# Optimization experiments

Hardware: AMD Instinct MI355X
Metric: run time of the kernel (lower is better)

Reference implementation:

```python
import jax, jax.numpy as jnp
import numpy as np

N_NODES = 50000
N_EDGES = 800000
D_IN = 256
D_HID = 128


def setup_inputs() -> dict:
    key = jax.random.key(0)
    ks = jax.random.split(key, 10)
    x = jax.random.normal(ks[0], (N_NODES, D_IN), dtype=jnp.float32)
    edge_index = jax.random.randint(ks[1], (2, N_EDGES), 0, N_NODES, dtype=jnp.int64)
    # GCNConv params (glorot-ish init), 3 layers: 256->128, 128->128, 128->128
    def glorot(k, fan_in, fan_out):
        s = jnp.sqrt(6.0 / (fan_in + fan_out))
        return jax.random.uniform(k, (fan_in, fan_out), jnp.float32, -s, s)
    W0 = glorot(ks[2], D_IN, D_HID)
    b0 = jnp.zeros((D_HID,), jnp.float32)
    W1 = glorot(ks[3], D_HID, D_HID)
    b1 = jnp.zeros((D_HID,), jnp.float32)
    W2 = glorot(ks[4], D_HID, D_HID)
    b2 = jnp.zeros((D_HID,), jnp.float32)
    return {"x": x, "edge_index": edge_index, "W0": W0, "b0": b0,
            "W1": W1, "b1": b1, "W2": W2, "b2": b2}


def _gcn_conv(x, W, b, src, dst, deg_inv_sqrt, deg_inv):
    # PyG GCNConv: x' = D^{-1/2} (A + I) D^{-1/2} (x W) + b
    h = x @ W  # [N, d_out]
    norm = deg_inv_sqrt[src] * deg_inv_sqrt[dst]  # [E]
    msg = h[src] * norm[:, None]  # gather + scale, [E, d_out]
    agg = jax.ops.segment_sum(msg, dst, num_segments=x.shape[0])
    # self-loop contribution: norm = deg^{-1/2} * deg^{-1/2} = 1/deg
    return agg + h * deg_inv[:, None] + b


def reference(x, edge_index, W0, b0, W1, b1, W2, b2):
    src, dst = edge_index[0], edge_index[1]
    n = x.shape[0]
    # degree with self loops (computed on destination, source_to_target flow)
    deg = jax.ops.segment_sum(jnp.ones((src.shape[0],), x.dtype), dst,
                              num_segments=n) + 1.0
    deg_inv_sqrt = deg ** -0.5
    deg_inv = 1.0 / deg
    h = jax.nn.relu(_gcn_conv(x, W0, b0, src, dst, deg_inv_sqrt, deg_inv))
    h = jax.nn.relu(_gcn_conv(h, W1, b1, src, dst, deg_inv_sqrt, deg_inv))
    h = jax.nn.relu(_gcn_conv(h, W2, b2, src, dst, deg_inv_sqrt, deg_inv))
    return h
```

## Files before the change

### kernel.cpp

```cpp
#include <hip/hip_runtime.h>

#define N_NODES 50000
#define N_EDGES 800000
#define D_HID   128

typedef unsigned int uint;
typedef unsigned short ushort;
typedef __attribute__((ext_vector_type(8))) short short8;
typedef __attribute__((ext_vector_type(4))) float f32x4;

#define NB       196
#define CAP      6144
#define P1_BLOCKS 200
#define P1_CHUNK  4000

__global__ __launch_bounds__(256) void part_k(const int* __restrict__ src,
                                              const int* __restrict__ dst,
                                              int* __restrict__ bcur,
                                              int2* __restrict__ ebuf, int e) {
    __shared__ int hist[NB];
    __shared__ int base[NB];
    int tid = threadIdx.x;
    if (tid < NB) hist[tid] = 0;
    __syncthreads();

    int e0 = blockIdx.x * P1_CHUNK;
    int2 ed[16];
    bool val[16];
#pragma unroll
    for (int i = 0; i < 16; ++i) {
        int o = i * 256 + tid;
        int idx = e0 + o;
        val[i] = (o < P1_CHUNK) && (idx < e);
        if (val[i]) {
            ed[i] = make_int2(src[idx], dst[idx]);
            atomicAdd(&hist[ed[i].y >> 8], 1);
        }
    }
    __syncthreads();
    if (tid < NB && hist[tid] > 0) base[tid] = atomicAdd(&bcur[tid], hist[tid]);
    __syncthreads();
    if (tid < NB) hist[tid] = 0;
    __syncthreads();
#pragma unroll
    for (int i = 0; i < 16; ++i) {
        if (val[i]) {
            int bk = ed[i].y >> 8;
            int o  = base[bk] + atomicAdd(&hist[bk], 1);
            if (o < CAP) ebuf[(size_t)bk * CAP + o] = ed[i];
        }
    }
}

__global__ void bscan196_k(const int* __restrict__ bcur, int* __restrict__ boff,
                           int* __restrict__ row_ptr_end) {
    __shared__ int s[256];
    int t = threadIdx.x;
    int v = (t < NB) ? bcur[t] : 0;
    s[t] = v;
    __syncthreads();
    for (int off = 1; off < 256; off <<= 1) {
        int u = (t >= off) ? s[t - off] : 0;
        __syncthreads();
        s[t] += u;
        __syncthreads();
    }
    if (t < NB) boff[t] = s[t] - v;
    if (t == 255) *row_ptr_end = s[255];
}

__global__ __launch_bounds__(256) void cntscan_k(const int2* __restrict__ ebuf,
                                                 const int* __restrict__ bcnt,
                                                 const int* __restrict__ boff,
                                                 int* __restrict__ row_ptr,
                                                 float* __restrict__ dis, int n) {
    __shared__ int c[256];
    __shared__ int s[256];
    int b = blockIdx.x, tid = threadIdx.x;
    c[tid] = 0;
    __syncthreads();
    int m = bcnt[b]; if (m > CAP) m = CAP;
    for (int i = tid; i < m; i += 256)
        atomicAdd(&c[ebuf[(size_t)b * CAP + i].y & 255], 1);
    __syncthreads();
    int v = c[tid];
    s[tid] = v;
    __syncthreads();
    for (int off = 1; off < 256; off <<= 1) {
        int u = (tid >= off) ? s[tid - off] : 0;
        __syncthreads();
        s[tid] += u;
        __syncthreads();
    }
    int node = b * 256 + tid;
    if (node < n) {
        row_ptr[node] = boff[b] + s[tid] - v;
        dis[node] = rsqrtf((float)v + 1.0f);
    }
}

__global__ __launch_bounds__(256) void csr_k(const int2* __restrict__ ebuf,
                                             const int* __restrict__ bcnt,
                                             const int* __restrict__ row_ptr,
                                             int* __restrict__ col, int n) {
    __shared__ int rp_l[257];
    __shared__ int cur[256];
    __shared__ int win[CAP];
    int b = blockIdx.x, tid = threadIdx.x;
    int node0 = b * 256;
    for (int i = tid; i < 257; i += 256) {
        int nd = node0 + i; if (nd > n) nd = n;
        rp_l[i] = row_ptr[nd];
    }
    cur[tid] = 0;
    __syncthreads();
    int base0 = rp_l[0];
    int m = bcnt[b]; if (m > CAP) m = CAP;

    for (int i = tid; i < m; i += 256) {
        int2 ed = ebuf[(size_t)b * CAP + i];
        int ll = ed.y & 255;
        int pos = rp_l[ll] + atomicAdd(&cur[ll], 1) - base0;
        win[pos] = ed.x << 8;
    }
    __syncthreads();
    for (int i = tid; i < m; i += 256) col[base0 + i] = win[i];
}

__global__ __launch_bounds__(256) void rowsort_k(const int* __restrict__ rp,
                                                 int* __restrict__ col, int n) {
    int node = blockIdx.x * 4 + (threadIdx.x >> 6);
    if (node >= n) return;
    int lane = threadIdx.x & 63;
    int beg = rp[node], end = rp[node + 1];
    int len = end - beg;
    if (len <= 1) return;
    if (len <= 64) {
        int v = (lane < len) ? col[beg + lane] : 0x7fffffff;
#pragma unroll
        for (int k = 2; k <= 64; k <<= 1)
#pragma unroll
            for (int j = k >> 1; j > 0; j >>= 1) {
                int other = __shfl_xor(v, j);
                bool up    = (lane & k) == 0;
                bool small = (lane & j) == 0;
                v = (small == up) ? min(v, other) : max(v, other);
            }
        if (lane < len) col[beg + lane] = v;
    } else if (lane == 0) {
        for (int i = beg + 1; i < end; ++i) {
            int key = col[i]; int j = i - 1;
            while (j >= beg && col[j] > key) { col[j + 1] = col[j]; --j; }
            col[j + 1] = key;
        }
    }
}

__device__ inline ushort f2bf(float f) {
    unsigned u = __float_as_uint(f);
    unsigned rounding = 0x7fffu + ((u >> 16) & 1u);
    return (ushort)((u + rounding) >> 16);
}
__device__ inline float bf_lo(uint v) { return __uint_as_float(v << 16); }
__device__ inline float bf_hi(uint v) { return __uint_as_float(v & 0xffff0000u); }
__device__ inline short8 cvt8(float4 f0, float4 f1) {
    short8 r;
    r[0] = (short)f2bf(f0.x); r[1] = (short)f2bf(f0.y);
    r[2] = (short)f2bf(f0.z); r[3] = (short)f2bf(f0.w);
    r[4] = (short)f2bf(f1.x); r[5] = (short)f2bf(f1.y);
    r[6] = (short)f2bf(f1.z); r[7] = (short)f2bf(f1.w);
    return r;
}

__device__ inline void gload16(const void* g, void* l) {
    __builtin_amdgcn_global_load_lds(
        (const __attribute__((address_space(1))) uint*)g,
        (__attribute__((address_space(3))) uint*)l, 16, 0, 0);
}

__global__ void wtrans_all_k(const float* __restrict__ W0, const float* __restrict__ W1,
                             const float* __restrict__ W2, ushort* __restrict__ Wt0,
                             ushort* __restrict__ Wt1, ushort* __restrict__ Wt2,
                             uint* __restrict__ hb_padrow) {
    int i = blockIdx.x * 256 + threadIdx.x;
    if (i < 64) hb_padrow[i] = 0;
    const float* W; ushort* Wt; int K, j;
    if (i < 32768)      { W = W0; Wt = Wt0; K = 256; j = i; }
    else if (i < 49152) { W = W1; Wt = Wt1; K = 128; j = i - 32768; }
    else                { W = W2; Wt = Wt2; K = 128; j = i - 49152; }
    int k = j >> 7, n = j & 127;
    Wt[(size_t)n * K + k] = f2bf(W[j]);
}

template<int K, int ROWS, bool AF32>
__global__ __launch_bounds__(256) void gemm_lds_k(const void* __restrict__ Ap,
                                                  const ushort* __restrict__ Bt,
                                                  const float* __restrict__ dis,
                                                  ushort* __restrict__ H,
                                                  int M) {
    constexpr int T  = K / 32;
    constexpr int EB = AF32 ? 4 : 2;
    constexpr int RS = K * EB;
    constexpr int NI = (ROWS * RS) / 4096;
    __shared__ char As[ROWS * RS];

    int tid = threadIdx.x;
    int w = tid >> 6, l = tid & 63, lr = l & 15, hi = l >> 4;
    int cBase = w * 32;

    short8 b[2][T];
#pragma unroll
    for (int c = 0; c < 2; ++c)
#pragma unroll
        for (int t = 0; t < T; ++t)
            b[c][t] = *(const short8*)&Bt[(size_t)(cBase + c * 16 + lr) * K + t * 32 + hi * 8];

    int r0 = blockIdx.x * ROWS;
    const char* gbase = (const char*)Ap + (size_t)r0 * RS;

#pragma unroll
    for (int i = 0; i < NI; ++i) {
        int L0  = (i * 4 + w) * 1024;
        int L   = L0 + l * 16;
        int row = L / RS;
        int cb  = (L % RS) >> 4;
        int gb  = (cb ^ (row & 7)) << 4;
        int grow = (r0 + row < M) ? row : 0;
        gload16(gbase + (size_t)grow * RS + gb, &As[L0]);
    }
    __syncthreads();

    f32x4 acc[ROWS / 16][2];
#pragma unroll
    for (int rb = 0; rb < ROWS / 16; ++rb)
#pragma unroll
        for (int c = 0; c < 2; ++c) acc[rb][c] = (f32x4){0.f, 0.f, 0.f, 0.f};

#pragma unroll
    for (int rb = 0; rb < ROWS / 16; ++rb) {
        int row = rb * 16 + lr;
        int s = row & 7;
        const char* rbase = &As[row * RS];
#pragma unroll
        for (int t = 0; t < T; ++t) {
            short8 a;
            if constexpr (AF32) {
                int cb0 = t * 8 + hi * 2;
                float4 f0 = *(const float4*)(rbase + ((cb0 ^ s) << 4));
                float4 f1 = *(const float4*)(rbase + (((cb0 + 1) ^ s) << 4));
                a = cvt8(f0, f1);
            } else {
                int cb0 = t * 4 + hi;
                a = *(const short8*)(rbase + ((cb0 ^ s) << 4));
            }
#pragma unroll
            for (int c = 0; c < 2; ++c)
                acc[rb][c] = __builtin_amdgcn_mfma_f32_16x16x32_bf16(a, b[c][t], acc[rb][c], 0, 0, 0);
        }
    }

#pragma unroll
    for (int rb = 0; rb < ROWS / 16; ++rb) {
#pragma unroll
        for (int j = 0; j < 4; ++j) {
            int r = r0 + rb * 16 + hi * 4 + j;
            if (r < M) {
                float d = dis[r];
#pragma unroll
                for (int c = 0; c < 2; ++c)
                    H[(size_t)r * 128 + cBase + c * 16 + lr] = f2bf(acc[rb][c][j] * d);
            }
        }
    }
}

template<bool LAST>
__global__ __launch_bounds__(256) void aggregate_k(const ushort* __restrict__ hs,
                                                   const int* __restrict__ row_ptr,
                                                   const int* __restrict__ col,
                                                   const float* __restrict__ dis,
                                                   const float* __restrict__ bias,
                                                   ushort* __restrict__ act,
                                                   float* __restrict__ out, int n) {
    int node = blockIdx.x * 4 + (threadIdx.x >> 6);
    if (node >= n) return;
    int lane = threadIdx.x & 63;
    int g  = lane >> 4;
    int cl = lane & 15;
    const char* base = (const char*)hs + (cl << 4);

    float ax[8];
#pragma unroll
    for (int j = 0; j < 8; ++j) ax[j] = 0.f;

    int beg = row_ptr[node], end = row_ptr[node + 1];
    for (int e = beg; e < end; e += 32) {
        int s[8];
#pragma unroll
        for (int q = 0; q < 8; ++q) {
            int idx = e + q * 4 + g;
            s[q] = (idx < end) ? col[idx] : (N_NODES << 8);
        }
        uint4 u[8];
#pragma unroll
        for (int q = 0; q < 8; ++q)
            u[q] = *(const uint4*)(base + (size_t)(uint)s[q]);
#pragma unroll
        for (int q = 0; q < 8; ++q) {
            ax[0] += bf_lo(u[q].x); ax[1] += bf_hi(u[q].x);
            ax[2] += bf_lo(u[q].y); ax[3] += bf_hi(u[q].y);
            ax[4] += bf_lo(u[q].z); ax[5] += bf_hi(u[q].z);
            ax[6] += bf_lo(u[q].w); ax[7] += bf_hi(u[q].w);
        }
    }
#pragma unroll
    for (int j = 0; j < 8; ++j) {
        ax[j] += __shfl_xor(ax[j], 16);
        ax[j] += __shfl_xor(ax[j], 32);
    }
    if (g == 0) {
        float dn = dis[node];
        uint4 un = *(const uint4*)(base + ((size_t)node << 8));
        float hsn[8] = {bf_lo(un.x), bf_hi(un.x), bf_lo(un.y), bf_hi(un.y),
                        bf_lo(un.z), bf_hi(un.z), bf_lo(un.w), bf_hi(un.w)};
        int c0 = cl * 8;
        float4 bv0 = *(const float4*)&bias[c0];
        float4 bv1 = *(const float4*)&bias[c0 + 4];
        float bb[8] = {bv0.x, bv0.y, bv0.z, bv0.w, bv1.x, bv1.y, bv1.z, bv1.w};
        float o[8];
#pragma unroll
        for (int j = 0; j < 8; ++j)
            o[j] = fmaxf((ax[j] + hsn[j]) * dn + bb[j], 0.f);
        if (LAST) {
            *(float4*)&out[(size_t)node * D_HID + c0]     = make_float4(o[0], o[1], o[2], o[3]);
            *(float4*)&out[(size_t)node * D_HID + c0 + 4] = make_float4(o[4], o[5], o[6], o[7]);
        } else {
            uint4 p;
            p.x = (uint)f2bf(o[0]) | ((uint)f2bf(o[1]) << 16);
            p.y = (uint)f2bf(o[2]) | ((uint)f2bf(o[3]) << 16);
            p.z = (uint)f2bf(o[4]) | ((uint)f2bf(o[5]) << 16);
            p.w = (uint)f2bf(o[6]) | ((uint)f2bf(o[7]) << 16);
            *(uint4*)((char*)act + ((size_t)node << 8) + (cl << 4)) = p;
        }
    }
}

extern "C" void kernel_launch(void* const* d_in, const int* in_sizes, int n_in,
                              void* d_out, int out_size, void* d_ws, size_t ws_size,
                              hipStream_t stream) {
    const float* x  = (const float*)d_in[0];
    const int*   ei = (const int*)d_in[1];
    const float* W0 = (const float*)d_in[2];
    const float* b0 = (const float*)d_in[3];
    const float* W1 = (const float*)d_in[4];
    const float* b1 = (const float*)d_in[5];
    const float* W2 = (const float*)d_in[6];
    const float* b2 = (const float*)d_in[7];
    float* out = (float*)d_out;

    const int N = N_NODES, E = N_EDGES;
    const int* src = ei;
    const int* dst = ei + E;

    char* w = (char*)d_ws;
    size_t off = 0;
    auto alloc = [&](size_t bytes) {
        size_t o = off;
        off += (bytes + 255) & ~(size_t)255;
        return o;
    };
    int*    bcur   = (int*)(w + alloc((size_t)NB * 4));
    float*  dis    = (float*)(w + alloc((size_t)N * 4));
    int*    rp     = (int*)(w + alloc((size_t)(N + 1) * 4));
    int*    boff   = (int*)(w + alloc((size_t)NB * 4));
    int*    col    = (int*)(w + alloc((size_t)E * 4));
    int2*   ebuf   = (int2*)(w + alloc((size_t)NB * CAP * 8));
    ushort* hb     = (ushort*)(w + alloc((size_t)(N + 1) * D_HID * 2));
    ushort* act    = (ushort*)(w + alloc((size_t)N * D_HID * 2));
    ushort* Wt0    = (ushort*)(w + alloc((size_t)128 * 256 * 2));
    ushort* Wt1    = (ushort*)(w + alloc((size_t)128 * 128 * 2));
    ushort* Wt2    = (ushort*)(w + alloc((size_t)128 * 128 * 2));
    (void)ws_size; (void)n_in; (void)in_sizes; (void)out_size;

    hipMemsetAsync(bcur, 0, (size_t)NB * 4, stream);

    part_k<<<P1_BLOCKS, 256, 0, stream>>>(src, dst, bcur, ebuf, E);
    bscan196_k<<<1, 256, 0, stream>>>(bcur, boff, rp + N);
    cntscan_k<<<NB, 256, 0, stream>>>(ebuf, bcur, boff, rp, dis, N);
    csr_k<<<NB, 256, 0, stream>>>(ebuf, bcur, rp, col, N);
    rowsort_k<<<(N + 3) / 4, 256, 0, stream>>>(rp, col, N);

    wtrans_all_k<<<256, 256, 0, stream>>>(W0, W1, W2, Wt0, Wt1, Wt2,
                                          (uint*)(hb + (size_t)N * D_HID));

    int g32 = (N + 31) / 32;
    int g64 = (N + 63) / 64;
    int agg_grid = (N + 3) / 4;

    gemm_lds_k<256, 32, true><<<g32, 256, 0, stream>>>(x, Wt0, dis, hb, N);
    aggregate_k<false><<<agg_grid, 256, 0, stream>>>(hb, rp, col, dis, b0, act, out, N);
    gemm_lds_k<128, 64, false><<<g64, 256, 0, stream>>>(act, Wt1, dis, hb, N);
    aggregate_k<false><<<agg_grid, 256, 0, stream>>>(hb, rp, col, dis, b1, act, out, N);
    gemm_lds_k<128, 64, false><<<g64, 256, 0, stream>>>(act, Wt2, dis, hb, N);
    aggregate_k<true><<<agg_grid, 256, 0, stream>>>(hb, rp, col, dis, b2, act, out, N);
}
```

Baseline: 230.2 us.

## Fuse degree count and CSR fill; split aggregation feature dim across two blocks

Merges the count/scan kernel and CSR placement kernel into one, computing local offsets in LDS so one launch and a second pass over ebuf/row_ptr disappear. The aggregation kernel now splits the 128 feature columns into two 64-column halves handled by separate blocks, each wave covering 8 edges per step with 8 lanes per row, which doubles the grid and the number of edges in flight per wave. The cost is that col indices are read twice and there is an extra shuffle reduction step.

```diff
diff --git a/kernel.cpp b/kernel.cpp
--- a/kernel.cpp
+++ b/kernel.cpp
@@ -69,61 +69,49 @@
     if (t == 255) *row_ptr_end = s[255];
 }
 
-__global__ __launch_bounds__(256) void cntscan_k(const int2* __restrict__ ebuf,
-                                                 const int* __restrict__ bcnt,
-                                                 const int* __restrict__ boff,
-                                                 int* __restrict__ row_ptr,
-                                                 float* __restrict__ dis, int n) {
-    __shared__ int c[256];
-    __shared__ int s[256];
-    int b = blockIdx.x, tid = threadIdx.x;
-    c[tid] = 0;
-    __syncthreads();
-    int m = bcnt[b]; if (m > CAP) m = CAP;
-    for (int i = tid; i < m; i += 256)
-        atomicAdd(&c[ebuf[(size_t)b * CAP + i].y & 255], 1);
-    __syncthreads();
-    int v = c[tid];
-    s[tid] = v;
-    __syncthreads();
-    for (int off = 1; off < 256; off <<= 1) {
-        int u = (tid >= off) ? s[tid - off] : 0;
-        __syncthreads();
-        s[tid] += u;
-        __syncthreads();
-    }
-    int node = b * 256 + tid;
-    if (node < n) {
-        row_ptr[node] = boff[b] + s[tid] - v;
-        dis[node] = rsqrtf((float)v + 1.0f);
-    }
-}
-
-__global__ __launch_bounds__(256) void csr_k(const int2* __restrict__ ebuf,
-                                             const int* __restrict__ bcnt,
-                                             const int* __restrict__ row_ptr,
-                                             int* __restrict__ col, int n) {
-    __shared__ int rp_l[257];
+__global__ __launch_bounds__(256) void csr2_k(const int2* __restrict__ ebuf,
+                                              const int* __restrict__ bcnt,
+                                              const int* __restrict__ boff,
+                                              int* __restrict__ row_ptr,
+                                              float* __restrict__ dis,
+                                              int* __restrict__ col, int n) {
+    __shared__ int deg[256];
+    __shared__ int loc[256];
     __shared__ int cur[256];
     __shared__ int win[CAP];
     int b = blockIdx.x, tid = threadIdx.x;
-    int node0 = b * 256;
-    for (int i = tid; i < 257; i += 256) {
-        int nd = node0 + i; if (nd > n) nd = n;
-        rp_l[i] = row_ptr[nd];
-    }
-    cur[tid] = 0;
-    __syncthreads();
-    int base0 = rp_l[0];
+    deg[tid] = 0; cur[tid] = 0;
+    __syncthreads();
     int m = bcnt[b]; if (m > CAP) m = CAP;
-
+    const int2* eb = ebuf + (size_t)b * CAP;
+    for (int i = tid; i < m; i += 256)
+        atomicAdd(&deg[eb[i].y & 255], 1);
+    __syncthreads();
+    int v = deg[tid];
+    loc[tid] = v;
+    __syncthreads();
+    for (int off = 1; off < 256; off <<= 1) {
+        int u = (tid >= off) ? loc[tid - off] : 0;
+        __syncthreads();
+        loc[tid] += u;
+        __syncthreads();
+    }
+    int excl = loc[tid] - v;
+    int node = b * 256 + tid;
+    if (node < n) {
+        row_ptr[node] = boff[b] + excl;
+        dis[node] = rsqrtf((float)v + 1.0f);
+    }
+    loc[tid] = excl;
+    __syncthreads();
     for (int i = tid; i < m; i += 256) {
-        int2 ed = ebuf[(size_t)b * CAP + i];
+        int2 ed = eb[i];
         int ll = ed.y & 255;
-        int pos = rp_l[ll] + atomicAdd(&cur[ll], 1) - base0;
+        int pos = loc[ll] + atomicAdd(&cur[ll], 1);
         win[pos] = ed.x << 8;
     }
     __syncthreads();
+    int base0 = boff[b];
     for (int i = tid; i < m; i += 256) col[base0 + i] = win[i];
 }
 
@@ -281,13 +269,17 @@
                                                    const float* __restrict__ dis,
                                                    const float* __restrict__ bias,
                                                    ushort* __restrict__ act,
-                                                   float* __restrict__ out, int n) {
-    int node = blockIdx.x * 4 + (threadIdx.x >> 6);
+                                                   float* __restrict__ out,
+                                                   int n, int halfG) {
+    int bid  = blockIdx.x;
+    int half = (bid >= halfG) ? 1 : 0;
+    int nb   = bid - half * halfG;
+    int node = nb * 4 + (threadIdx.x >> 6);
     if (node >= n) return;
     int lane = threadIdx.x & 63;
-    int g  = lane >> 4;
-    int cl = lane & 15;
-    const char* base = (const char*)hs + (cl << 4);
+    int g  = lane >> 3;
+    int cl = lane & 7;
+    const char* base = (const char*)hs + half * 128 + (cl << 4);
 
     float ax[8];
 #pragma unroll
@@ -295,18 +287,18 @@
 
     int beg = row_ptr[node], end = row_ptr[node + 1];
     for (int e = beg; e < end; e += 32) {
-        int s[8];
-#pragma unroll
-        for (int q = 0; q < 8; ++q) {
-            int idx = e + q * 4 + g;
+        int s[4];
+#pragma unroll
+        for (int q = 0; q < 4; ++q) {
+            int idx = e + q * 8 + g;
             s[q] = (idx < end) ? col[idx] : (N_NODES << 8);
         }
-        uint4 u[8];
-#pragma unroll
-        for (int q = 0; q < 8; ++q)
+        uint4 u[4];
+#pragma unroll
+        for (int q = 0; q < 4; ++q)
             u[q] = *(const uint4*)(base + (size_t)(uint)s[q]);
 #pragma unroll
-        for (int q = 0; q < 8; ++q) {
+        for (int q = 0; q < 4; ++q) {
             ax[0] += bf_lo(u[q].x); ax[1] += bf_hi(u[q].x);
             ax[2] += bf_lo(u[q].y); ax[3] += bf_hi(u[q].y);
             ax[4] += bf_lo(u[q].z); ax[5] += bf_hi(u[q].z);
@@ -315,6 +307,7 @@
     }
 #pragma unroll
     for (int j = 0; j < 8; ++j) {
+        ax[j] += __shfl_xor(ax[j], 8);
         ax[j] += __shfl_xor(ax[j], 16);
         ax[j] += __shfl_xor(ax[j], 32);
     }
@@ -323,7 +316,7 @@
         uint4 un = *(const uint4*)(base + ((size_t)node << 8));
         float hsn[8] = {bf_lo(un.x), bf_hi(un.x), bf_lo(un.y), bf_hi(un.y),
                         bf_lo(un.z), bf_hi(un.z), bf_lo(un.w), bf_hi(un.w)};
-        int c0 = cl * 8;
+        int c0 = half * 64 + cl * 8;
         float4 bv0 = *(const float4*)&bias[c0];
         float4 bv1 = *(const float4*)&bias[c0 + 4];
         float bb[8] = {bv0.x, bv0.y, bv0.z, bv0.w, bv1.x, bv1.y, bv1.z, bv1.w};
@@ -340,7 +333,7 @@
             p.y = (uint)f2bf(o[2]) | ((uint)f2bf(o[3]) << 16);
             p.z = (uint)f2bf(o[4]) | ((uint)f2bf(o[5]) << 16);
             p.w = (uint)f2bf(o[6]) | ((uint)f2bf(o[7]) << 16);
-            *(uint4*)((char*)act + ((size_t)node << 8) + (cl << 4)) = p;
+            *(uint4*)((char*)act + ((size_t)node << 8) + half * 128 + (cl << 4)) = p;
         }
     }
 }
@@ -386,8 +379,7 @@
 
     part_k<<<P1_BLOCKS, 256, 0, stream>>>(src, dst, bcur, ebuf, E);
     bscan196_k<<<1, 256, 0, stream>>>(bcur, boff, rp + N);
-    cntscan_k<<<NB, 256, 0, stream>>>(ebuf, bcur, boff, rp, dis, N);
-    csr_k<<<NB, 256, 0, stream>>>(ebuf, bcur, rp, col, N);
+    csr2_k<<<NB, 256, 0, stream>>>(ebuf, bcur, boff, rp, dis, col, N);
     rowsort_k<<<(N + 3) / 4, 256, 0, stream>>>(rp, col, N);
 
     wtrans_all_k<<<256, 256, 0, stream>>>(W0, W1, W2, Wt0, Wt1, Wt2,
@@ -395,12 +387,13 @@
 
     int g32 = (N + 31) / 32;
     int g64 = (N + 63) / 64;
-    int agg_grid = (N + 3) / 4;
+    int halfG = (N + 3) / 4;
+    int agg_grid = 2 * halfG;
 
     gemm_lds_k<256, 32, true><<<g32, 256, 0, stream>>>(x, Wt0, dis, hb, N);
-    aggregate_k<false><<<agg_grid, 256, 0, stream>>>(hb, rp, col, dis, b0, act, out, N);
+    aggregate_k<false><<<agg_grid, 256, 0, stream>>>(hb, rp, col, dis, b0, act, out, N, halfG);
     gemm_lds_k<128, 64, false><<<g64, 256, 0, stream>>>(act, Wt1, dis, hb, N);
-    aggregate_k<false><<<agg_grid, 256, 0, stream>>>(hb, rp, col, dis, b1, act, out, N);
+    aggregate_k<false><<<agg_grid, 256, 0, stream>>>(hb, rp, col, dis, b1, act, out, N, halfG);
     gemm_lds_k<128, 64, false><<<g64, 256, 0, stream>>>(act, Wt2, dis, hb, N);
-    aggregate_k<true><<<agg_grid, 256, 0, stream>>>(hb, rp, col, dis, b2, act, out, N);
-}
+    aggregate_k<true><<<agg_grid, 256, 0, stream>>>(hb, rp, col, dis, b2, act, out, N, halfG);
+}
```

New measurement: 230.7 us. No clear change (+0.2%).
